# Kernel tuning notes

Measured on AMD Instinct MI355X. Metric: run time of the kernel, lower is better.

## Reference

```python
import jax, jax.numpy as jnp
import numpy as np

NUM_CLUSTERS = 64
DIM = 128
ALPHA = 100.0


def setup_inputs() -> dict:
    key = jax.random.key(0)
    k1, k2 = jax.random.split(key)
    x = jax.random.normal(k1, (32, 4096, DIM), dtype=jnp.float32)
    centroids = jax.random.uniform(k2, (NUM_CLUSTERS, DIM), dtype=jnp.float32)
    return {"x": x, "centroids": centroids}


def reference(x, centroids):
    # x: [B, N, D], centroids: [K, D]
    # Euclidean distances (torch.cdist p=2): [B, N, K]
    x2 = jnp.sum(x * x, axis=-1, keepdims=True)            # [B, N, 1]
    c2 = jnp.sum(centroids * centroids, axis=-1)            # [K]
    xc = jnp.einsum('bnd,kd->bnk', x, centroids)            # [B, N, K]
    dist2 = jnp.maximum(x2 + c2[None, None, :] - 2.0 * xc, 0.0)
    distances = jnp.sqrt(dist2)
    soft_assign = jax.nn.softmax(-ALPHA * distances, axis=2)  # [B, N, K]
    # vlad[b,k,:] = sum_n a[b,n,k] * (x[b,n,:] - c[k,:])
    vlad = jnp.einsum('bnk,bnd->bkd', soft_assign, x) \
         - jnp.sum(soft_assign, axis=1)[:, :, None] * centroids[None, :, :]
    B = x.shape[0]
    vlad = vlad.reshape(B, -1)
    # F.normalize(p=2, dim=1) with default eps=1e-12
    norm = jnp.maximum(jnp.linalg.norm(vlad, axis=1, keepdims=True), 1e-12)
    return vlad / norm
```

## Files before the change

kernel.cpp:

```cpp
#include <hip/hip_runtime.h>

typedef _Float16 half8 __attribute__((ext_vector_type(8)));
typedef _Float16 half4_t __attribute__((ext_vector_type(4)));
typedef float floatx4 __attribute__((ext_vector_type(4)));

static constexpr int NB  = 32;
static constexpr int NP  = 4096;
static constexpr int DD  = 128;
static constexpr int KC  = 64;
static constexpr int TN  = 64;
static constexpr int TPB = 4;
static constexpr int SCP = 136;
static constexpr int STP = 72;

#define ALPHA_  100.0f
#define LOG2E_  1.44269504088896f

__global__ __launch_bounds__(256, 3)
void vlad_phase1(const float* __restrict__ xg, const float* __restrict__ cg,
                 float* __restrict__ vlad, float* __restrict__ colsum)
{
    __shared__ __align__(16) _Float16 sxt[DD][STP];
    __shared__ __align__(16) _Float16 sat[KC][STP];
    __shared__ __align__(16) _Float16 sclo[KC][SCP];
    __shared__ float sc2[KC];

    const int tid  = threadIdx.x;
    const int lane = tid & 63;
    const int w    = tid >> 6;
    const int l15  = lane & 15;
    const int quad = lane >> 4;
    const int b    = blockIdx.y;
    const float* xb = xg + (size_t)b * NP * DD;

    half8 chi[4][4];
#pragma unroll
    for (int mt = 0; mt < 4; ++mt)
#pragma unroll
        for (int ks = 0; ks < 4; ++ks) {
            const float* p = cg + (mt*16 + l15)*DD + ks*32 + quad*8;
            float4 a  = *(const float4*)p;
            float4 bb = *(const float4*)(p + 4);
            half8 h;
            h[0]=(_Float16)a.x;  h[1]=(_Float16)a.y;  h[2]=(_Float16)a.z;  h[3]=(_Float16)a.w;
            h[4]=(_Float16)bb.x; h[5]=(_Float16)bb.y; h[6]=(_Float16)bb.z; h[7]=(_Float16)bb.w;
            chi[mt][ks] = h;
        }
    {
        int k = tid >> 2, qq = tid & 3;
        const float* rp = cg + k*DD + qq*32;
        float c2p = 0.f;
#pragma unroll
        for (int j = 0; j < 8; ++j) {
            float4 v = *(const float4*)(rp + j*4);
            c2p += v.x*v.x + v.y*v.y + v.z*v.z + v.w*v.w;
            half4_t lo;
            lo[0] = (_Float16)(v.x - (float)(_Float16)v.x);
            lo[1] = (_Float16)(v.y - (float)(_Float16)v.y);
            lo[2] = (_Float16)(v.z - (float)(_Float16)v.z);
            lo[3] = (_Float16)(v.w - (float)(_Float16)v.w);
            *(half4_t*)&sclo[k][(qq*8 + j)*4] = lo;
        }
        c2p += __shfl_xor(c2p, 1);
        c2p += __shfl_xor(c2p, 2);
        if (qq == 0) sc2[k] = c2p;
    }
    __syncthreads();

    floatx4 acc2[8];
#pragma unroll
    for (int i = 0; i < 8; ++i) acc2[i] = (floatx4){0.f, 0.f, 0.f, 0.f};
    floatx4 accs = (floatx4){0.f, 0.f, 0.f, 0.f};

    half8 onesf;
#pragma unroll
    for (int j = 0; j < 8; ++j) onesf[j] = (_Float16)((l15 == 0) ? 1.0f : 0.0f);

    const int nloc = w*16 + l15;
    const int scol = nloc ^ (quad << 4);

    for (int tt = 0; tt < TPB; ++tt) {
        const int n0 = (blockIdx.x * TPB + tt) * TN;
        const float* xrow = xb + (size_t)(n0 + nloc) * DD + quad*8;

        float4 fa[4], fb[4];
#pragma unroll
        for (int ks = 0; ks < 4; ++ks) {
            fa[ks] = *(const float4*)(xrow + ks*32);
            fb[ks] = *(const float4*)(xrow + ks*32 + 4);
        }

        float ssq = 0.f;
        floatx4 acc1[4];
#pragma unroll
        for (int mt = 0; mt < 4; ++mt) acc1[mt] = (floatx4){0.f, 0.f, 0.f, 0.f};

#pragma unroll
        for (int ks = 0; ks < 4; ++ks) {
            half8 xf;
            xf[0]=(_Float16)fa[ks].x; xf[1]=(_Float16)fa[ks].y;
            xf[2]=(_Float16)fa[ks].z; xf[3]=(_Float16)fa[ks].w;
            xf[4]=(_Float16)fb[ks].x; xf[5]=(_Float16)fb[ks].y;
            xf[6]=(_Float16)fb[ks].z; xf[7]=(_Float16)fb[ks].w;
            ssq += fa[ks].x*fa[ks].x + fa[ks].y*fa[ks].y + fa[ks].z*fa[ks].z + fa[ks].w*fa[ks].w
                 + fb[ks].x*fb[ks].x + fb[ks].y*fb[ks].y + fb[ks].z*fb[ks].z + fb[ks].w*fb[ks].w;
#pragma unroll
            for (int j = 0; j < 8; ++j)
                sxt[ks*32 + quad*8 + j][scol] = xf[j];
#pragma unroll
            for (int mt = 0; mt < 4; ++mt) {
                half8 cl = *(const half8*)&sclo[mt*16 + l15][ks*32 + quad*8];
                acc1[mt] = __builtin_amdgcn_mfma_f32_16x16x32_f16(chi[mt][ks], xf, acc1[mt], 0, 0, 0);
                acc1[mt] = __builtin_amdgcn_mfma_f32_16x16x32_f16(cl,          xf, acc1[mt], 0, 0, 0);
            }
        }
        ssq += __shfl_xor(ssq, 16);
        ssq += __shfl_xor(ssq, 32);

        float dist[4][4];
#pragma unroll
        for (int mt = 0; mt < 4; ++mt) {
            floatx4 c2v = *(const floatx4*)&sc2[mt*16 + quad*4];
#pragma unroll
            for (int r = 0; r < 4; ++r) {
                float d2 = ssq + c2v[r] - 2.f*acc1[mt][r];
                dist[mt][r] = sqrtf(fmaxf(d2, 0.f));
            }
        }
        float dmin = dist[0][0];
#pragma unroll
        for (int mt = 0; mt < 4; ++mt)
#pragma unroll
            for (int r = 0; r < 4; ++r) dmin = fminf(dmin, dist[mt][r]);
        dmin = fminf(dmin, __shfl_xor(dmin, 16));
        dmin = fminf(dmin, __shfl_xor(dmin, 32));
        float pv[4][4];
        float psum = 0.f;
#pragma unroll
        for (int mt = 0; mt < 4; ++mt)
#pragma unroll
            for (int r = 0; r < 4; ++r) {
                float e = exp2f((dmin - dist[mt][r]) * (ALPHA_ * LOG2E_));
                pv[mt][r] = e; psum += e;
            }
        psum += __shfl_xor(psum, 16);
        psum += __shfl_xor(psum, 32);
        float invs = 1.0f / psum;
#pragma unroll
        for (int mt = 0; mt < 4; ++mt)
#pragma unroll
            for (int r = 0; r < 4; ++r) {
                sat[mt*16 + quad*4 + r][scol] = (_Float16)(pv[mt][r] * invs);
            }
        __syncthreads();

#pragma unroll
        for (int ks2 = 0; ks2 < 2; ++ks2) {
            const int nbase = ks2*32 + quad*8;
            half8 af = *(const half8*)&sat[w*16 + l15][nbase ^ ((l15 >> 2) << 4)];
            accs = __builtin_amdgcn_mfma_f32_16x16x32_f16(af, onesf, accs, 0, 0, 0);
#pragma unroll
            for (int nt = 0; nt < 8; ++nt) {
                const int d = nt*16 + l15;
                half8 bf = *(const half8*)&sxt[d][nbase ^ (((d >> 3) & 3) << 4)];
                acc2[nt] = __builtin_amdgcn_mfma_f32_16x16x32_f16(af, bf, acc2[nt], 0, 0, 0);
            }
        }
        __syncthreads();
    }

#pragma unroll
    for (int nt = 0; nt < 8; ++nt)
#pragma unroll
        for (int r = 0; r < 4; ++r) {
            int k = w*16 + quad*4 + r;
            int d = nt*16 + l15;
            atomicAdd(&vlad[((size_t)b*KC + k)*DD + d], acc2[nt][r]);
        }
    if (l15 == 0) {
#pragma unroll
        for (int r = 0; r < 4; ++r)
            atomicAdd(&colsum[b*KC + w*16 + quad*4 + r], accs[r]);
    }
}

__global__ __launch_bounds__(256)
void vlad_finalize(const float* __restrict__ vlad, const float* __restrict__ colsum,
                   const float* __restrict__ cg, float* __restrict__ out)
{
    __shared__ float red[4];
    const int b = blockIdx.x;
    const int tid = threadIdx.x;
    float v[32];
    float ss = 0.f;
#pragma unroll
    for (int i = 0; i < 32; ++i) {
        int idx = i*256 + tid;
        float val = vlad[(size_t)b*8192 + idx] - colsum[b*64 + (idx >> 7)] * cg[idx];
        v[i] = val;
        ss += val * val;
    }
#pragma unroll
    for (int m = 1; m < 64; m <<= 1) ss += __shfl_xor(ss, m);
    if ((tid & 63) == 0) red[tid >> 6] = ss;
    __syncthreads();
    float tot = red[0] + red[1] + red[2] + red[3];
    float scale = 1.0f / fmaxf(sqrtf(tot), 1e-12f);
#pragma unroll
    for (int i = 0; i < 32; ++i)
        out[(size_t)b*8192 + i*256 + tid] = v[i] * scale;
}

extern "C" void kernel_launch(void* const* d_in, const int* in_sizes, int n_in,
                              void* d_out, int out_size, void* d_ws, size_t ws_size,
                              hipStream_t stream)
{
    (void)in_sizes; (void)n_in; (void)out_size; (void)ws_size;
    const float* x = (const float*)d_in[0];
    const float* c = (const float*)d_in[1];
    float* out  = (float*)d_out;
    float* vlad = (float*)d_ws;
    float* cs   = vlad + (size_t)NB*KC*DD;

    hipMemsetAsync(d_ws, 0, (size_t)(NB*KC*DD + NB*KC) * sizeof(float), stream);
    vlad_phase1<<<dim3(16, 32), 256, 0, stream>>>(x, c, vlad, cs);
    vlad_finalize<<<32, 256, 0, stream>>>(vlad, cs, c, out);
}
```

Before: 128.8 us.

## Fuse finalize into main kernel via last-block counter, prefetch next tile

Merges the normalization kernel into the accumulation kernel: each block increments a per-batch counter after its atomics, and the last block for a batch reads the accumulated VLAD and colsum with atomic loads, then normalizes and writes the output. It also halves tiles per block, doubling the grid to 1024 blocks, and register-prefetches the next x tile while the current one is processed. This removes one kernel launch and spreads work over more CUs, at the cost of twice as many atomic adds into the VLAD buffer and a serialized tail in the last block of each batch.

```diff
diff --git a/kernel.cpp b/kernel.cpp
--- a/kernel.cpp
+++ b/kernel.cpp
@@ -9,7 +9,8 @@
 static constexpr int DD  = 128;
 static constexpr int KC  = 64;
 static constexpr int TN  = 64;
-static constexpr int TPB = 4;
+static constexpr int TPB = 2;
+static constexpr int BPB = NP / (TPB * TN);
 static constexpr int SCP = 136;
 static constexpr int STP = 72;
 
@@ -17,13 +18,16 @@
 #define LOG2E_  1.44269504088896f
 
 __global__ __launch_bounds__(256, 3)
-void vlad_phase1(const float* __restrict__ xg, const float* __restrict__ cg,
-                 float* __restrict__ vlad, float* __restrict__ colsum)
+void vlad_fused(const float* __restrict__ xg, const float* __restrict__ cg,
+                float* __restrict__ vlad, float* __restrict__ colsum,
+                int* __restrict__ cnt, float* __restrict__ out)
 {
     __shared__ __align__(16) _Float16 sxt[DD][STP];
     __shared__ __align__(16) _Float16 sat[KC][STP];
     __shared__ __align__(16) _Float16 sclo[KC][SCP];
     __shared__ float sc2[KC];
+    __shared__ float red[4];
+    __shared__ int   isLastS;
 
     const int tid  = threadIdx.x;
     const int lane = tid & 63;
@@ -78,40 +82,56 @@
 
     const int nloc = w*16 + l15;
     const int scol = nloc ^ (quad << 4);
-
+    const float* xpt = xb + (size_t)(blockIdx.x*TPB*TN + nloc)*DD + quad*8;
+
+    float4 fa[4], fb[4];
+#pragma unroll
+    for (int ks = 0; ks < 4; ++ks) {
+        fa[ks] = *(const float4*)(xpt + ks*32);
+        fb[ks] = *(const float4*)(xpt + ks*32 + 4);
+    }
+
+#pragma unroll
     for (int tt = 0; tt < TPB; ++tt) {
-        const int n0 = (blockIdx.x * TPB + tt) * TN;
-        const float* xrow = xb + (size_t)(n0 + nloc) * DD + quad*8;
-
-        float4 fa[4], fb[4];
+        half8 xf[4];
+        float ssq = 0.f;
 #pragma unroll
         for (int ks = 0; ks < 4; ++ks) {
-            fa[ks] = *(const float4*)(xrow + ks*32);
-            fb[ks] = *(const float4*)(xrow + ks*32 + 4);
-        }
-
-        float ssq = 0.f;
-        floatx4 acc1[4];
-#pragma unroll
-        for (int mt = 0; mt < 4; ++mt) acc1[mt] = (floatx4){0.f, 0.f, 0.f, 0.f};
-
-#pragma unroll
-        for (int ks = 0; ks < 4; ++ks) {
-            half8 xf;
-            xf[0]=(_Float16)fa[ks].x; xf[1]=(_Float16)fa[ks].y;
-            xf[2]=(_Float16)fa[ks].z; xf[3]=(_Float16)fa[ks].w;
-            xf[4]=(_Float16)fb[ks].x; xf[5]=(_Float16)fb[ks].y;
-            xf[6]=(_Float16)fb[ks].z; xf[7]=(_Float16)fb[ks].w;
+            half8 h;
+            h[0]=(_Float16)fa[ks].x; h[1]=(_Float16)fa[ks].y;
+            h[2]=(_Float16)fa[ks].z; h[3]=(_Float16)fa[ks].w;
+            h[4]=(_Float16)fb[ks].x; h[5]=(_Float16)fb[ks].y;
+            h[6]=(_Float16)fb[ks].z; h[7]=(_Float16)fb[ks].w;
+            xf[ks] = h;
             ssq += fa[ks].x*fa[ks].x + fa[ks].y*fa[ks].y + fa[ks].z*fa[ks].z + fa[ks].w*fa[ks].w
                  + fb[ks].x*fb[ks].x + fb[ks].y*fb[ks].y + fb[ks].z*fb[ks].z + fb[ks].w*fb[ks].w;
+        }
+
+        if (tt + 1 < TPB) {
+            const float* xr = xpt + (size_t)(tt + 1) * TN * DD;
+#pragma unroll
+            for (int ks = 0; ks < 4; ++ks) {
+                fa[ks] = *(const float4*)(xr + ks*32);
+                fb[ks] = *(const float4*)(xr + ks*32 + 4);
+            }
+        }
+
+#pragma unroll
+        for (int ks = 0; ks < 4; ++ks)
 #pragma unroll
             for (int j = 0; j < 8; ++j)
-                sxt[ks*32 + quad*8 + j][scol] = xf[j];
+                sxt[ks*32 + quad*8 + j][scol] = xf[ks][j];
+
+        floatx4 acc1[4];
+#pragma unroll
+        for (int mt = 0; mt < 4; ++mt) acc1[mt] = (floatx4){0.f, 0.f, 0.f, 0.f};
+#pragma unroll
+        for (int ks = 0; ks < 4; ++ks) {
 #pragma unroll
             for (int mt = 0; mt < 4; ++mt) {
                 half8 cl = *(const half8*)&sclo[mt*16 + l15][ks*32 + quad*8];
-                acc1[mt] = __builtin_amdgcn_mfma_f32_16x16x32_f16(chi[mt][ks], xf, acc1[mt], 0, 0, 0);
-                acc1[mt] = __builtin_amdgcn_mfma_f32_16x16x32_f16(cl,          xf, acc1[mt], 0, 0, 0);
+                acc1[mt] = __builtin_amdgcn_mfma_f32_16x16x32_f16(chi[mt][ks], xf[ks], acc1[mt], 0, 0, 0);
+                acc1[mt] = __builtin_amdgcn_mfma_f32_16x16x32_f16(cl,          xf[ks], acc1[mt], 0, 0, 0);
             }
         }
         ssq += __shfl_xor(ssq, 16);
@@ -149,9 +169,8 @@
 #pragma unroll
         for (int mt = 0; mt < 4; ++mt)
 #pragma unroll
-            for (int r = 0; r < 4; ++r) {
+            for (int r = 0; r < 4; ++r)
                 sat[mt*16 + quad*4 + r][scol] = (_Float16)(pv[mt][r] * invs);
-            }
         __syncthreads();
 
 #pragma unroll
@@ -182,21 +201,26 @@
         for (int r = 0; r < 4; ++r)
             atomicAdd(&colsum[b*KC + w*16 + quad*4 + r], accs[r]);
     }
-}
-
-__global__ __launch_bounds__(256)
-void vlad_finalize(const float* __restrict__ vlad, const float* __restrict__ colsum,
-                   const float* __restrict__ cg, float* __restrict__ out)
-{
-    __shared__ float red[4];
-    const int b = blockIdx.x;
-    const int tid = threadIdx.x;
+
+    __threadfence();
+    if (tid == 0) {
+        int old = atomicAdd(&cnt[b], 1);
+        isLastS = (old == BPB - 1) ? 1 : 0;
+    }
+    __syncthreads();
+    if (!isLastS) return;
+    __threadfence();
+
     float v[32];
     float ss = 0.f;
 #pragma unroll
     for (int i = 0; i < 32; ++i) {
         int idx = i*256 + tid;
-        float val = vlad[(size_t)b*8192 + idx] - colsum[b*64 + (idx >> 7)] * cg[idx];
+        float vl = __hip_atomic_load(&vlad[(size_t)b*8192 + idx],
+                                     __ATOMIC_RELAXED, __HIP_MEMORY_SCOPE_AGENT);
+        float cv = __hip_atomic_load(&colsum[b*KC + (idx >> 7)],
+                                     __ATOMIC_RELAXED, __HIP_MEMORY_SCOPE_AGENT);
+        float val = vl - cv * cg[idx];
         v[i] = val;
         ss += val * val;
     }
@@ -221,8 +245,8 @@
     float* out  = (float*)d_out;
     float* vlad = (float*)d_ws;
     float* cs   = vlad + (size_t)NB*KC*DD;
-
-    hipMemsetAsync(d_ws, 0, (size_t)(NB*KC*DD + NB*KC) * sizeof(float), stream);
-    vlad_phase1<<<dim3(16, 32), 256, 0, stream>>>(x, c, vlad, cs);
-    vlad_finalize<<<32, 256, 0, stream>>>(vlad, cs, c, out);
+    int*   cnt  = (int*)(cs + (size_t)NB*KC);
+
+    hipMemsetAsync(d_ws, 0, (size_t)(NB*KC*DD + NB*KC + NB) * sizeof(float), stream);
+    vlad_fused<<<dim3(NP/(TPB*TN), NB), 256, 0, stream>>>(x, c, vlad, cs, cnt, out);
 }
```

Result: slower. 278.1 us (+115.9%).
